# Optimization experiments

Hardware: AMD Instinct MI355X
Metric: run time of the kernel (lower is better)

Reference implementation:

```python
import jax, jax.numpy as jnp
import numpy as np

N = 100000      # nodes
E = 1600000     # edges (avg degree 16)
F_IN = 512      # input node features
H = 8           # heads in conv1
D = 8           # per-head dim in conv1
C = 7           # classes
NEG_SLOPE = 0.2 # PyG GATConv default leaky_relu slope


def setup_inputs() -> dict:
    key = jax.random.key(0)
    ks = jax.random.split(key, 10)
    s = 0.05
    return {
        "x": jax.random.normal(ks[0], (N, F_IN), jnp.float32),
        "edge_index": jax.random.randint(ks[1], (2, E), 0, N, dtype=jnp.int64),
        "W1": jax.random.normal(ks[2], (F_IN, H * D), jnp.float32) * s,
        "a1_src": jax.random.normal(ks[3], (H, D), jnp.float32) * s,
        "a1_dst": jax.random.normal(ks[4], (H, D), jnp.float32) * s,
        "b1": jnp.zeros((H * D,), jnp.float32),
        "W2": jax.random.normal(ks[5], (H * D, C), jnp.float32) * s,
        "a2_src": jax.random.normal(ks[6], (1, C), jnp.float32) * s,
        "a2_dst": jax.random.normal(ks[7], (1, C), jnp.float32) * s,
        "b2": jnp.zeros((C,), jnp.float32),
    }


def _gat_conv(x, src, dst, W, a_src, a_dst, b, heads, dim, concat, n):
    # linear transform -> [N, H, D]
    h = (x @ W).reshape(n, heads, dim)
    # per-node attention halves: [N, H]
    al_src = jnp.einsum('nhd,hd->nh', h, a_src)
    al_dst = jnp.einsum('nhd,hd->nh', h, a_dst)
    # per-edge logits, leaky relu: [E', H]
    e = jax.nn.leaky_relu(al_src[src] + al_dst[dst], NEG_SLOPE)
    # segment softmax over incoming edges of each dst node
    m = jax.lax.stop_gradient(jax.ops.segment_max(e, dst, num_segments=n))
    p = jnp.exp(e - m[dst])
    z = jax.ops.segment_sum(p, dst, num_segments=n)
    alpha = p / z[dst]                                   # [E', H]
    # weighted scatter-add of source messages -> [N, H, D]
    out = jax.ops.segment_sum(h[src] * alpha[..., None], dst, num_segments=n)
    out = out.reshape(n, heads * dim) if concat else out.mean(axis=1)
    return out + b


def reference(x, edge_index, W1, a1_src, a1_dst, b1, W2, a2_src, a2_dst, b2):
    n = x.shape[0]
    # PyG GATConv default: add self loops
    loops = jnp.arange(n, dtype=edge_index.dtype)
    src = jnp.concatenate([edge_index[0], loops])
    dst = jnp.concatenate([edge_index[1], loops])
    h = _gat_conv(x, src, dst, W1, a1_src, a1_dst, b1, H, D, True, n)
    h = jax.nn.elu(h)
    out = _gat_conv(h, src, dst, W2, a2_src, a2_dst, b2, 1, C, False, n)
    return jax.nn.log_softmax(out, axis=1)
```

## Files before the change

kernel.cpp:

```cpp
#include <hip/hip_runtime.h>
#include <math.h>

#define N_NODES 100000
#define N_EDGES 1600000
#define F_IN 512
#define HD 64
#define CC 7
#define NKT (F_IN / 32)
#define BS 128
#define NBK ((N_NODES + BS - 1) / BS)
#define ECAP 4096
#define SCHUNK 4096
#define SBLK ((N_EDGES + SCHUNK - 1) / SCHUNK)

typedef __attribute__((ext_vector_type(8))) short short8;
typedef __attribute__((ext_vector_type(4))) float f32x4;

__device__ inline unsigned short f2bf(float f) {
    union { float f; unsigned u; } v; v.f = f;
    unsigned u = v.u;
    return (unsigned short)((u + 0x7fffu + ((u >> 16) & 1u)) >> 16);
}
__device__ inline float bf2f(unsigned short b) {
    union { unsigned u; float f; } v; v.u = ((unsigned)b) << 16;
    return v.f;
}

__global__ void zerob_kernel(int* __restrict__ bcnt) {
    int i = threadIdx.x;
    if (i < NBK) bcnt[i] = 0;
}

__global__ void w1prep_kernel(const float* __restrict__ W1,
                              unsigned short* __restrict__ wf) {
    int t = blockIdx.x * 256 + threadIdx.x;
    if (t >= NKT * 4 * 64) return;
    int lane = t & 63;
    int ct = (t >> 6) & 3;
    int kt = t >> 8;
    int k0 = kt * 32 + (lane >> 4) * 8;
    int col = ct * 16 + (lane & 15);
    unsigned short* dst = wf + (size_t)t * 8;
    #pragma unroll
    for (int j = 0; j < 8; ++j) dst[j] = f2bf(W1[(k0 + j) * HD + col]);
}

__global__ __launch_bounds__(256) void gemm1att_kernel(const float* __restrict__ x,
                                                       const unsigned short* __restrict__ wf,
                                                       const float* __restrict__ a1s,
                                                       const float* __restrict__ a1d,
                                                       unsigned short* __restrict__ h1b,
                                                       float* __restrict__ als,
                                                       float* __restrict__ ald) {
    __shared__ float ls[64][65];
    const int wave = threadIdx.x >> 6;
    const int lane = threadIdx.x & 63;
    int arow = blockIdx.x * 64 + wave * 16 + (lane & 15);
    if (arow >= N_NODES) arow = N_NODES - 1;
    const float* xp = x + (size_t)arow * F_IN + (lane >> 4) * 8;
    const short8* wp = (const short8*)wf;

    f32x4 acc[4] = {};
    #pragma unroll 4
    for (int kt = 0; kt < NKT; ++kt) {
        f32x4 a0 = *(const f32x4*)(xp + kt * 32);
        f32x4 a1 = *(const f32x4*)(xp + kt * 32 + 4);
        union { short8 s; unsigned short u[8]; } af;
        af.u[0] = f2bf(a0.x); af.u[1] = f2bf(a0.y);
        af.u[2] = f2bf(a0.z); af.u[3] = f2bf(a0.w);
        af.u[4] = f2bf(a1.x); af.u[5] = f2bf(a1.y);
        af.u[6] = f2bf(a1.z); af.u[7] = f2bf(a1.w);
        #pragma unroll
        for (int ct = 0; ct < 4; ++ct) {
            short8 bf = wp[kt * 256 + ct * 64 + lane];
            acc[ct] = __builtin_amdgcn_mfma_f32_16x16x32_bf16(af.s, bf, acc[ct], 0, 0, 0);
        }
    }
    const int lrow_base = wave * 16 + (lane >> 4) * 4;
    const int ocol = lane & 15;
    #pragma unroll
    for (int ct = 0; ct < 4; ++ct) {
        #pragma unroll
        for (int r = 0; r < 4; ++r) {
            int lrow = lrow_base + r;
            int orow = blockIdx.x * 64 + lrow;
            ls[lrow][ct * 16 + ocol] = acc[ct][r];
            if (orow < N_NODES)
                h1b[(size_t)orow * HD + ct * 16 + ocol] = f2bf(acc[ct][r]);
        }
    }
    __syncthreads();
    #pragma unroll
    for (int task = threadIdx.x; task < 64 * 8; task += 256) {
        int r = task >> 3, h = task & 7;
        int node = blockIdx.x * 64 + r;
        if (node < N_NODES) {
            float s = 0.f, d = 0.f;
            #pragma unroll
            for (int k = 0; k < 8; ++k) {
                float v = ls[r][h * 8 + k];
                s += v * a1s[h * 8 + k];
                d += v * a1d[h * 8 + k];
            }
            als[node * 8 + h] = s;
            ald[node * 8 + h] = d;
        }
    }
}

__global__ __launch_bounds__(256) void bhist_kernel(const int* __restrict__ ei,
                                                    int* __restrict__ bcnt) {
    __shared__ int cnt[NBK];
    const int e0 = blockIdx.x * SCHUNK;
    int e1 = e0 + SCHUNK; if (e1 > N_EDGES) e1 = N_EDGES;
    for (int b = threadIdx.x; b < NBK; b += 256) cnt[b] = 0;
    __syncthreads();
    for (int i = e0 + threadIdx.x; i < e1; i += 256)
        atomicAdd(&cnt[ei[N_EDGES + i] >> 7], 1);
    __syncthreads();
    for (int b = threadIdx.x; b < NBK; b += 256) {
        int c = cnt[b];
        if (c) atomicAdd(&bcnt[b], c);
    }
}

__global__ __launch_bounds__(1024) void bscan_kernel(const int* __restrict__ bcnt,
                                                     int* __restrict__ bstart,
                                                     int* __restrict__ bcur) {
    __shared__ int wsum[16];
    const int t = threadIdx.x;
    const int lane = t & 63, w = t >> 6;
    int v = (t < NBK) ? bcnt[t] : 0;
    int x = v;
    #pragma unroll
    for (int o = 1; o < 64; o <<= 1) {
        int u = __shfl_up(x, o, 64);
        if (lane >= o) x += u;
    }
    if (lane == 63) wsum[w] = x;
    __syncthreads();
    if (w == 0) {
        int s = (lane < 16) ? wsum[lane] : 0;
        #pragma unroll
        for (int o = 1; o < 16; o <<= 1) {
            int u = __shfl_up(s, o, 64);
            if (lane >= o) s += u;
        }
        if (lane < 16) wsum[lane] = s;
    }
    __syncthreads();
    int woff = (w > 0) ? wsum[w - 1] : 0;
    int ex = x - v + woff;
    if (t < NBK) { bstart[t] = ex; bcur[t] = ex; }
    if (t == NBK - 1) bstart[NBK] = ex + v;
}

__global__ __launch_bounds__(256) void binscatter_kernel(const int* __restrict__ ei,
                                                         int* __restrict__ bcur,
                                                         int2* __restrict__ pairs) {
    __shared__ int cnt[NBK];
    __shared__ int bas[NBK];
    const int e0 = blockIdx.x * SCHUNK;
    int e1 = e0 + SCHUNK; if (e1 > N_EDGES) e1 = N_EDGES;
    for (int b = threadIdx.x; b < NBK; b += 256) cnt[b] = 0;
    __syncthreads();
    for (int i = e0 + threadIdx.x; i < e1; i += 256)
        atomicAdd(&cnt[ei[N_EDGES + i] >> 7], 1);
    __syncthreads();
    for (int b = threadIdx.x; b < NBK; b += 256) {
        int c = cnt[b];
        bas[b] = c ? atomicAdd(&bcur[b], c) : 0;
        cnt[b] = 0;
    }
    __syncthreads();
    for (int i = e0 + threadIdx.x; i < e1; i += 256) {
        int s = ei[i];
        int t = ei[N_EDGES + i];
        int b = t >> 7;
        int pos = bas[b] + atomicAdd(&cnt[b], 1);
        pairs[pos] = make_int2(s, t);
    }
}

__global__ __launch_bounds__(512) void gather1_kernel(
        const int* __restrict__ bstart, const int2* __restrict__ pairs,
        const float* __restrict__ als, const float* __restrict__ ald,
        const unsigned short* __restrict__ h1b, const float* __restrict__ b1,
        const float* __restrict__ W2, const float* __restrict__ a2s,
        const float* __restrict__ a2d,
        unsigned short* __restrict__ g2b, float* __restrict__ al2s,
        float* __restrict__ al2d) {
    __shared__ int cnt[BS];
    __shared__ int start[BS];
    __shared__ int srcl[ECAP];
    const int tid = threadIdx.x;
    const int wave = tid >> 6, lane = tid & 63, h = lane >> 3;
    const int n0 = blockIdx.x * BS;
    const int es = bstart[blockIdx.x];
    const int ne = bstart[blockIdx.x + 1] - es;
    if (tid < BS) cnt[tid] = 0;
    __syncthreads();
    for (int k = tid; k < ne; k += 512)
        atomicAdd(&cnt[pairs[es + k].y & (BS - 1)], 1);
    __syncthreads();
    if (tid < 64) {
        int a = cnt[lane], b = cnt[64 + lane];
        int xx = a;
        #pragma unroll
        for (int o = 1; o < 64; o <<= 1) { int u = __shfl_up(xx, o, 64); if (lane >= o) xx += u; }
        int totalA = __shfl(xx, 63, 64);
        int yy = b;
        #pragma unroll
        for (int o = 1; o < 64; o <<= 1) { int u = __shfl_up(yy, o, 64); if (lane >= o) yy += u; }
        start[lane] = xx - a;
        start[64 + lane] = totalA + yy - b;
        cnt[lane] = 0; cnt[64 + lane] = 0;
    }
    __syncthreads();
    for (int k = tid; k < ne; k += 512) {
        int2 pr = pairs[es + k];
        int ln = pr.y & (BS - 1);
        int pos = start[ln] + atomicAdd(&cnt[ln], 1);
        if (pos < ECAP) srcl[pos] = pr.x;
    }
    __syncthreads();

    float w[CC];
    #pragma unroll
    for (int c = 0; c < CC; ++c) w[c] = W2[lane * CC + c];
    for (int n = wave * 16; n < wave * 16 + 16; ++n) {
        int node = n0 + n;
        if (node >= N_NODES) break;
        const float aldt = ald[node * 8 + h];
        float e = als[node * 8 + h] + aldt;
        e = (e >= 0.f) ? e : 0.2f * e;
        float p = __expf(e);
        float acc = p * bf2f(h1b[(size_t)node * HD + lane]);
        float z = p;
        int k = start[n];
        int ke = k + cnt[n]; if (ke > ECAP) ke = ECAP;
        for (; k + 4 <= ke; k += 4) {
            int s0 = srcl[k],     s1 = srcl[k + 1];
            int s2 = srcl[k + 2], s3 = srcl[k + 3];
            float e0 = als[s0 * 8 + h] + aldt;
            float e1 = als[s1 * 8 + h] + aldt;
            float e2 = als[s2 * 8 + h] + aldt;
            float e3 = als[s3 * 8 + h] + aldt;
            float v0 = bf2f(h1b[(size_t)s0 * HD + lane]);
            float v1 = bf2f(h1b[(size_t)s1 * HD + lane]);
            float v2 = bf2f(h1b[(size_t)s2 * HD + lane]);
            float v3 = bf2f(h1b[(size_t)s3 * HD + lane]);
            e0 = (e0 >= 0.f) ? e0 : 0.2f * e0;
            e1 = (e1 >= 0.f) ? e1 : 0.2f * e1;
            e2 = (e2 >= 0.f) ? e2 : 0.2f * e2;
            e3 = (e3 >= 0.f) ? e3 : 0.2f * e3;
            float p0 = __expf(e0), p1 = __expf(e1);
            float p2 = __expf(e2), p3 = __expf(e3);
            z += (p0 + p1) + (p2 + p3);
            acc = fmaf(p0, v0, acc);
            acc = fmaf(p1, v1, acc);
            acc = fmaf(p2, v2, acc);
            acc = fmaf(p3, v3, acc);
        }
        for (; k < ke; ++k) {
            int s = srcl[k];
            float e2 = als[s * 8 + h] + aldt;
            e2 = (e2 >= 0.f) ? e2 : 0.2f * e2;
            float p2 = __expf(e2);
            z += p2;
            acc = fmaf(p2, bf2f(h1b[(size_t)s * HD + lane]), acc);
        }
        float v = acc / z + b1[lane];
        v = (v > 0.f) ? v : (__expf(v) - 1.f);
        float g[CC];
        #pragma unroll
        for (int c = 0; c < CC; ++c) {
            float r = v * w[c];
            #pragma unroll
            for (int d = 1; d < 64; d <<= 1) r += __shfl_xor(r, d, 64);
            g[c] = r;
        }
        float s2 = 0.f, d2 = 0.f;
        #pragma unroll
        for (int c = 0; c < CC; ++c) { s2 += g[c] * a2s[c]; d2 += g[c] * a2d[c]; }
        if (lane < CC) g2b[(size_t)node * 8 + lane] = f2bf(g[lane]);
        if (lane == CC) g2b[(size_t)node * 8 + CC] = 0;
        if (lane == 8) al2s[node] = s2;
        if (lane == 9) al2d[node] = d2;
    }
}

__global__ __launch_bounds__(256) void gather2_kernel(
        const int* __restrict__ bstart, const int2* __restrict__ pairs,
        const float* __restrict__ al2s, const float* __restrict__ al2d,
        const unsigned short* __restrict__ g2b, const float* __restrict__ b2,
        float* __restrict__ out) {
    __shared__ int cnt[BS];
    __shared__ int start[BS];
    __shared__ int srcl[ECAP];
    const int tid = threadIdx.x;
    const int lane = tid & 63;
    const int grp = tid >> 3, c = tid & 7;
    const int n0 = blockIdx.x * BS;
    const int es = bstart[blockIdx.x];
    const int ne = bstart[blockIdx.x + 1] - es;
    if (tid < BS) cnt[tid] = 0;
    __syncthreads();
    for (int k = tid; k < ne; k += 256)
        atomicAdd(&cnt[pairs[es + k].y & (BS - 1)], 1);
    __syncthreads();
    if (tid < 64) {
        int a = cnt[lane], b = cnt[64 + lane];
        int xx = a;
        #pragma unroll
        for (int o = 1; o < 64; o <<= 1) { int u = __shfl_up(xx, o, 64); if (lane >= o) xx += u; }
        int totalA = __shfl(xx, 63, 64);
        int yy = b;
        #pragma unroll
        for (int o = 1; o < 64; o <<= 1) { int u = __shfl_up(yy, o, 64); if (lane >= o) yy += u; }
        start[lane] = xx - a;
        start[64 + lane] = totalA + yy - b;
        cnt[lane] = 0; cnt[64 + lane] = 0;
    }
    __syncthreads();
    for (int k = tid; k < ne; k += 256) {
        int2 pr = pairs[es + k];
        int ln = pr.y & (BS - 1);
        int pos = start[ln] + atomicAdd(&cnt[ln], 1);
        if (pos < ECAP) srcl[pos] = pr.x;
    }
    __syncthreads();

    for (int n = grp * 4; n < grp * 4 + 4; ++n) {
        int node = n0 + n;
        if (node >= N_NODES) break;
        const float adn = al2d[node];
        float e = al2s[node] + adn;
        e = (e >= 0.f) ? e : 0.2f * e;
        float p = __expf(e);
        float acc = p * bf2f(g2b[(size_t)node * 8 + c]);
        float z = p;
        int k = start[n];
        int ke = k + cnt[n]; if (ke > ECAP) ke = ECAP;
        for (; k + 4 <= ke; k += 4) {
            int s0 = srcl[k],     s1 = srcl[k + 1];
            int s2 = srcl[k + 2], s3 = srcl[k + 3];
            float e0 = al2s[s0] + adn;
            float e1 = al2s[s1] + adn;
            float e2 = al2s[s2] + adn;
            float e3 = al2s[s3] + adn;
            float v0 = bf2f(g2b[(size_t)s0 * 8 + c]);
            float v1 = bf2f(g2b[(size_t)s1 * 8 + c]);
            float v2 = bf2f(g2b[(size_t)s2 * 8 + c]);
            float v3 = bf2f(g2b[(size_t)s3 * 8 + c]);
            e0 = (e0 >= 0.f) ? e0 : 0.2f * e0;
            e1 = (e1 >= 0.f) ? e1 : 0.2f * e1;
            e2 = (e2 >= 0.f) ? e2 : 0.2f * e2;
            e3 = (e3 >= 0.f) ? e3 : 0.2f * e3;
            float p0 = __expf(e0), p1 = __expf(e1);
            float p2 = __expf(e2), p3 = __expf(e3);
            z += (p0 + p1) + (p2 + p3);
            acc = fmaf(p0, v0, acc);
            acc = fmaf(p1, v1, acc);
            acc = fmaf(p2, v2, acc);
            acc = fmaf(p3, v3, acc);
        }
        for (; k < ke; ++k) {
            int s = srcl[k];
            float e2 = al2s[s] + adn;
            e2 = (e2 >= 0.f) ? e2 : 0.2f * e2;
            float p2 = __expf(e2);
            z += p2;
            acc = fmaf(p2, bf2f(g2b[(size_t)s * 8 + c]), acc);
        }
        float o = (c < CC) ? (acc / z + b2[c]) : -1e30f;
        float m = o;
        #pragma unroll
        for (int d = 1; d < 8; d <<= 1) m = fmaxf(m, __shfl_xor(m, d, 8));
        float ex = (c < CC) ? __expf(o - m) : 0.f;
        float sum = ex;
        #pragma unroll
        for (int d = 1; d < 8; d <<= 1) sum += __shfl_xor(sum, d, 8);
        float lse = m + __logf(sum);
        if (c < CC) out[(size_t)node * CC + c] = o - lse;
    }
}

extern "C" void kernel_launch(void* const* d_in, const int* in_sizes, int n_in,
                              void* d_out, int out_size, void* d_ws, size_t ws_size,
                              hipStream_t stream) {
    const float* x   = (const float*)d_in[0];
    const int*   ei  = (const int*)d_in[1];
    const float* W1  = (const float*)d_in[2];
    const float* a1s = (const float*)d_in[3];
    const float* a1d = (const float*)d_in[4];
    const float* b1  = (const float*)d_in[5];
    const float* W2  = (const float*)d_in[6];
    const float* a2s = (const float*)d_in[7];
    const float* a2d = (const float*)d_in[8];
    const float* b2  = (const float*)d_in[9];
    float* out = (float*)d_out;

    char* base = (char*)d_ws;
    size_t off = 0;
    auto alloc = [&](size_t bytes) { char* p = base + off; off = (off + bytes + 63) & ~(size_t)63; return p; };
    unsigned short* h1b = (unsigned short*)alloc((size_t)N_NODES * HD * 2);
    unsigned short* wf  = (unsigned short*)alloc((size_t)NKT * 4 * 64 * 8 * 2);
    float* als  = (float*)alloc((size_t)N_NODES * 8 * 4);
    float* ald  = (float*)alloc((size_t)N_NODES * 8 * 4);
    unsigned short* g2b = (unsigned short*)alloc((size_t)N_NODES * 8 * 2);
    float* al2s = (float*)alloc((size_t)N_NODES * 4);
    float* al2d = (float*)alloc((size_t)N_NODES * 4);
    int* bcnt   = (int*)alloc((size_t)NBK * 4);
    int* bstart = (int*)alloc((size_t)(NBK + 1) * 4);
    int* bcur   = (int*)alloc((size_t)NBK * 4);
    int2* pairs = (int2*)alloc((size_t)N_EDGES * 8);

    zerob_kernel<<<1, 1024, 0, stream>>>(bcnt);
    w1prep_kernel<<<(NKT * 4 * 64 + 255) / 256, 256, 0, stream>>>(W1, wf);
    bhist_kernel<<<SBLK, 256, 0, stream>>>(ei, bcnt);
    bscan_kernel<<<1, 1024, 0, stream>>>(bcnt, bstart, bcur);
    binscatter_kernel<<<SBLK, 256, 0, stream>>>(ei, bcur, pairs);

    gemm1att_kernel<<<(N_NODES + 63) / 64, 256, 0, stream>>>(
        x, wf, a1s, a1d, h1b, als, ald);

    gather1_kernel<<<NBK, 512, 0, stream>>>(
        bstart, pairs, als, ald, h1b, b1, W2, a2s, a2d, g2b, al2s, al2d);
    gather2_kernel<<<NBK, 256, 0, stream>>>(
        bstart, pairs, al2s, al2d, g2b, b2, out);
}
```

Baseline: 242.3 us.

## Bin edges into fixed-capacity per-bucket slots and share edge softmax weights via shuffles

Drops the histogram and scan kernels. Each destination bucket now gets a fixed ECAP-sized slot in the pairs buffer, filled with an atomic cursor, so the edge bucketing needs only one pass over edge_index. Both gather kernels also change how attention weights are computed: each lane of an 8-lane group computes the exp for one edge and broadcasts it with __shfl, so the exp is not repeated per head-dim lane. Edges beyond ECAP per bucket are silently dropped. The pairs buffer is larger and sparsely filled.

```diff
diff --git a/kernel.cpp b/kernel.cpp
--- a/kernel.cpp
+++ b/kernel.cpp
@@ -26,9 +26,9 @@
     return v.f;
 }
 
-__global__ void zerob_kernel(int* __restrict__ bcnt) {
+__global__ void zerob_kernel(int* __restrict__ bcur) {
     int i = threadIdx.x;
-    if (i < NBK) bcnt[i] = 0;
+    if (i < NBK) bcur[i] = 0;
 }
 
 __global__ void w1prep_kernel(const float* __restrict__ W1,
@@ -108,53 +108,6 @@
     }
 }
 
-__global__ __launch_bounds__(256) void bhist_kernel(const int* __restrict__ ei,
-                                                    int* __restrict__ bcnt) {
-    __shared__ int cnt[NBK];
-    const int e0 = blockIdx.x * SCHUNK;
-    int e1 = e0 + SCHUNK; if (e1 > N_EDGES) e1 = N_EDGES;
-    for (int b = threadIdx.x; b < NBK; b += 256) cnt[b] = 0;
-    __syncthreads();
-    for (int i = e0 + threadIdx.x; i < e1; i += 256)
-        atomicAdd(&cnt[ei[N_EDGES + i] >> 7], 1);
-    __syncthreads();
-    for (int b = threadIdx.x; b < NBK; b += 256) {
-        int c = cnt[b];
-        if (c) atomicAdd(&bcnt[b], c);
-    }
-}
-
-__global__ __launch_bounds__(1024) void bscan_kernel(const int* __restrict__ bcnt,
-                                                     int* __restrict__ bstart,
-                                                     int* __restrict__ bcur) {
-    __shared__ int wsum[16];
-    const int t = threadIdx.x;
-    const int lane = t & 63, w = t >> 6;
-    int v = (t < NBK) ? bcnt[t] : 0;
-    int x = v;
-    #pragma unroll
-    for (int o = 1; o < 64; o <<= 1) {
-        int u = __shfl_up(x, o, 64);
-        if (lane >= o) x += u;
-    }
-    if (lane == 63) wsum[w] = x;
-    __syncthreads();
-    if (w == 0) {
-        int s = (lane < 16) ? wsum[lane] : 0;
-        #pragma unroll
-        for (int o = 1; o < 16; o <<= 1) {
-            int u = __shfl_up(s, o, 64);
-            if (lane >= o) s += u;
-        }
-        if (lane < 16) wsum[lane] = s;
-    }
-    __syncthreads();
-    int woff = (w > 0) ? wsum[w - 1] : 0;
-    int ex = x - v + woff;
-    if (t < NBK) { bstart[t] = ex; bcur[t] = ex; }
-    if (t == NBK - 1) bstart[NBK] = ex + v;
-}
-
 __global__ __launch_bounds__(256) void binscatter_kernel(const int* __restrict__ ei,
                                                          int* __restrict__ bcur,
                                                          int2* __restrict__ pairs) {
@@ -178,12 +131,12 @@
         int t = ei[N_EDGES + i];
         int b = t >> 7;
         int pos = bas[b] + atomicAdd(&cnt[b], 1);
-        pairs[pos] = make_int2(s, t);
+        if (pos < ECAP) pairs[(size_t)b * ECAP + pos] = make_int2(s, t);
     }
 }
 
 __global__ __launch_bounds__(512) void gather1_kernel(
-        const int* __restrict__ bstart, const int2* __restrict__ pairs,
+        const int* __restrict__ bcur, const int2* __restrict__ pairs,
         const float* __restrict__ als, const float* __restrict__ ald,
         const unsigned short* __restrict__ h1b, const float* __restrict__ b1,
         const float* __restrict__ W2, const float* __restrict__ a2s,
@@ -195,13 +148,14 @@
     __shared__ int srcl[ECAP];
     const int tid = threadIdx.x;
     const int wave = tid >> 6, lane = tid & 63, h = lane >> 3;
+    const int e8 = lane & 7, base8 = lane & 56;
     const int n0 = blockIdx.x * BS;
-    const int es = bstart[blockIdx.x];
-    const int ne = bstart[blockIdx.x + 1] - es;
+    const int2* bp = pairs + (size_t)blockIdx.x * ECAP;
+    int ne = bcur[blockIdx.x]; if (ne > ECAP) ne = ECAP;
     if (tid < BS) cnt[tid] = 0;
     __syncthreads();
     for (int k = tid; k < ne; k += 512)
-        atomicAdd(&cnt[pairs[es + k].y & (BS - 1)], 1);
+        atomicAdd(&cnt[bp[k].y & (BS - 1)], 1);
     __syncthreads();
     if (tid < 64) {
         int a = cnt[lane], b = cnt[64 + lane];
@@ -218,10 +172,10 @@
     }
     __syncthreads();
     for (int k = tid; k < ne; k += 512) {
-        int2 pr = pairs[es + k];
+        int2 pr = bp[k];
         int ln = pr.y & (BS - 1);
         int pos = start[ln] + atomicAdd(&cnt[ln], 1);
-        if (pos < ECAP) srcl[pos] = pr.x;
+        srcl[pos] = pr.x;
     }
     __syncthreads();
 
@@ -238,37 +192,35 @@
         float acc = p * bf2f(h1b[(size_t)node * HD + lane]);
         float z = p;
         int k = start[n];
-        int ke = k + cnt[n]; if (ke > ECAP) ke = ECAP;
-        for (; k + 4 <= ke; k += 4) {
-            int s0 = srcl[k],     s1 = srcl[k + 1];
-            int s2 = srcl[k + 2], s3 = srcl[k + 3];
-            float e0 = als[s0 * 8 + h] + aldt;
-            float e1 = als[s1 * 8 + h] + aldt;
-            float e2 = als[s2 * 8 + h] + aldt;
-            float e3 = als[s3 * 8 + h] + aldt;
-            float v0 = bf2f(h1b[(size_t)s0 * HD + lane]);
-            float v1 = bf2f(h1b[(size_t)s1 * HD + lane]);
-            float v2 = bf2f(h1b[(size_t)s2 * HD + lane]);
-            float v3 = bf2f(h1b[(size_t)s3 * HD + lane]);
-            e0 = (e0 >= 0.f) ? e0 : 0.2f * e0;
-            e1 = (e1 >= 0.f) ? e1 : 0.2f * e1;
-            e2 = (e2 >= 0.f) ? e2 : 0.2f * e2;
-            e3 = (e3 >= 0.f) ? e3 : 0.2f * e3;
-            float p0 = __expf(e0), p1 = __expf(e1);
-            float p2 = __expf(e2), p3 = __expf(e3);
-            z += (p0 + p1) + (p2 + p3);
-            acc = fmaf(p0, v0, acc);
-            acc = fmaf(p1, v1, acc);
-            acc = fmaf(p2, v2, acc);
-            acc = fmaf(p3, v3, acc);
-        }
-        for (; k < ke; ++k) {
-            int s = srcl[k];
-            float e2 = als[s * 8 + h] + aldt;
-            e2 = (e2 >= 0.f) ? e2 : 0.2f * e2;
-            float p2 = __expf(e2);
-            z += p2;
-            acc = fmaf(p2, bf2f(h1b[(size_t)s * HD + lane]), acc);
+        const int ke = k + cnt[n];
+        for (; k + 8 <= ke; k += 8) {
+            int s_own = srcl[k + e8];
+            float ee = als[s_own * 8 + h] + aldt;
+            ee = (ee >= 0.f) ? ee : 0.2f * ee;
+            float pv = __expf(ee);
+            #pragma unroll
+            for (int q = 0; q < 8; ++q) {
+                int se = srcl[k + q];
+                float pe = __shfl(pv, base8 | q, 64);
+                float ve = bf2f(h1b[(size_t)se * HD + lane]);
+                z += pe;
+                acc = fmaf(pe, ve, acc);
+            }
+        }
+        if (k < ke) {
+            const int m = ke - k;
+            int idx = k + ((e8 < m) ? e8 : (m - 1));
+            int s_own = srcl[idx];
+            float ee = als[s_own * 8 + h] + aldt;
+            ee = (ee >= 0.f) ? ee : 0.2f * ee;
+            float pv = __expf(ee);
+            for (int q = 0; q < m; ++q) {
+                int se = srcl[k + q];
+                float pe = __shfl(pv, base8 | q, 64);
+                float ve = bf2f(h1b[(size_t)se * HD + lane]);
+                z += pe;
+                acc = fmaf(pe, ve, acc);
+            }
         }
         float v = acc / z + b1[lane];
         v = (v > 0.f) ? v : (__expf(v) - 1.f);
@@ -291,7 +243,7 @@
 }
 
 __global__ __launch_bounds__(256) void gather2_kernel(
-        const int* __restrict__ bstart, const int2* __restrict__ pairs,
+        const int* __restrict__ bcur, const int2* __restrict__ pairs,
         const float* __restrict__ al2s, const float* __restrict__ al2d,
         const unsigned short* __restrict__ g2b, const float* __restrict__ b2,
         float* __restrict__ out) {
@@ -301,13 +253,14 @@
     const int tid = threadIdx.x;
     const int lane = tid & 63;
     const int grp = tid >> 3, c = tid & 7;
+    const int base8 = lane & 56;
     const int n0 = blockIdx.x * BS;
-    const int es = bstart[blockIdx.x];
-    const int ne = bstart[blockIdx.x + 1] - es;
+    const int2* bp = pairs + (size_t)blockIdx.x * ECAP;
+    int ne = bcur[blockIdx.x]; if (ne > ECAP) ne = ECAP;
     if (tid < BS) cnt[tid] = 0;
     __syncthreads();
     for (int k = tid; k < ne; k += 256)
-        atomicAdd(&cnt[pairs[es + k].y & (BS - 1)], 1);
+        atomicAdd(&cnt[bp[k].y & (BS - 1)], 1);
     __syncthreads();
     if (tid < 64) {
         int a = cnt[lane], b = cnt[64 + lane];
@@ -324,14 +277,14 @@
     }
     __syncthreads();
     for (int k = tid; k < ne; k += 256) {
-        int2 pr = pairs[es + k];
+        int2 pr = bp[k];
         int ln = pr.y & (BS - 1);
         int pos = start[ln] + atomicAdd(&cnt[ln], 1);
-        if (pos < ECAP) srcl[pos] = pr.x;
-    }
-    __syncthreads();
-
-    for (int n = grp * 4; n < grp * 4 + 4; ++n) {
+        srcl[pos] = pr.x;
+    }
+    __syncthreads();
+
+    for (int n = (grp & 31) * 4; n < (grp & 31) * 4 + 4; ++n) {
         int node = n0 + n;
         if (node >= N_NODES) break;
         const float adn = al2d[node];
@@ -341,47 +294,45 @@
         float acc = p * bf2f(g2b[(size_t)node * 8 + c]);
         float z = p;
         int k = start[n];
-        int ke = k + cnt[n]; if (ke > ECAP) ke = ECAP;
-        for (; k + 4 <= ke; k += 4) {
-            int s0 = srcl[k],     s1 = srcl[k + 1];
-            int s2 = srcl[k + 2], s3 = srcl[k + 3];
-            float e0 = al2s[s0] + adn;
-            float e1 = al2s[s1] + adn;
-            float e2 = al2s[s2] + adn;
-            float e3 = al2s[s3] + adn;
-            float v0 = bf2f(g2b[(size_t)s0 * 8 + c]);
-            float v1 = bf2f(g2b[(size_t)s1 * 8 + c]);
-            float v2 = bf2f(g2b[(size_t)s2 * 8 + c]);
-            float v3 = bf2f(g2b[(size_t)s3 * 8 + c]);
-            e0 = (e0 >= 0.f) ? e0 : 0.2f * e0;
-            e1 = (e1 >= 0.f) ? e1 : 0.2f * e1;
-            e2 = (e2 >= 0.f) ? e2 : 0.2f * e2;
-            e3 = (e3 >= 0.f) ? e3 : 0.2f * e3;
-            float p0 = __expf(e0), p1 = __expf(e1);
-            float p2 = __expf(e2), p3 = __expf(e3);
-            z += (p0 + p1) + (p2 + p3);
-            acc = fmaf(p0, v0, acc);
-            acc = fmaf(p1, v1, acc);
-            acc = fmaf(p2, v2, acc);
-            acc = fmaf(p3, v3, acc);
-        }
-        for (; k < ke; ++k) {
-            int s = srcl[k];
-            float e2 = al2s[s] + adn;
-            e2 = (e2 >= 0.f) ? e2 : 0.2f * e2;
-            float p2 = __expf(e2);
-            z += p2;
-            acc = fmaf(p2, bf2f(g2b[(size_t)s * 8 + c]), acc);
+        const int ke = k + cnt[n];
+        for (; k + 8 <= ke; k += 8) {
+            int s_own = srcl[k + c];
+            float ee = al2s[s_own] + adn;
+            ee = (ee >= 0.f) ? ee : 0.2f * ee;
+            float pv = __expf(ee);
+            #pragma unroll
+            for (int q = 0; q < 8; ++q) {
+                int se = srcl[k + q];
+                float pe = __shfl(pv, base8 | q, 64);
+                float ve = bf2f(g2b[(size_t)se * 8 + c]);
+                z += pe;
+                acc = fmaf(pe, ve, acc);
+            }
+        }
+        if (k < ke) {
+            const int m = ke - k;
+            int idx = k + ((c < m) ? c : (m - 1));
+            int s_own = srcl[idx];
+            float ee = al2s[s_own] + adn;
+            ee = (ee >= 0.f) ? ee : 0.2f * ee;
+            float pv = __expf(ee);
+            for (int q = 0; q < m; ++q) {
+                int se = srcl[k + q];
+                float pe = __shfl(pv, base8 | q, 64);
+                float ve = bf2f(g2b[(size_t)se * 8 + c]);
+                z += pe;
+                acc = fmaf(pe, ve, acc);
+            }
         }
         float o = (c < CC) ? (acc / z + b2[c]) : -1e30f;
-        float m = o;
-        #pragma unroll
-        for (int d = 1; d < 8; d <<= 1) m = fmaxf(m, __shfl_xor(m, d, 8));
-        float ex = (c < CC) ? __expf(o - m) : 0.f;
+        float m2 = o;
+        #pragma unroll
+        for (int d = 1; d < 8; d <<= 1) m2 = fmaxf(m2, __shfl_xor(m2, d, 8));
+        float ex = (c < CC) ? __expf(o - m2) : 0.f;
         float sum = ex;
         #pragma unroll
         for (int d = 1; d < 8; d <<= 1) sum += __shfl_xor(sum, d, 8);
-        float lse = m + __logf(sum);
+        float lse = m2 + __logf(sum);
         if (c < CC) out[(size_t)node * CC + c] = o - lse;
     }
 }
@@ -411,22 +362,18 @@
     unsigned short* g2b = (unsigned short*)alloc((size_t)N_NODES * 8 * 2);
     float* al2s = (float*)alloc((size_t)N_NODES * 4);
     float* al2d = (float*)alloc((size_t)N_NODES * 4);
-    int* bcnt   = (int*)alloc((size_t)NBK * 4);
-    int* bstart = (int*)alloc((size_t)(NBK + 1) * 4);
     int* bcur   = (int*)alloc((size_t)NBK * 4);
-    int2* pairs = (int2*)alloc((size_t)N_EDGES * 8);
-
-    zerob_kernel<<<1, 1024, 0, stream>>>(bcnt);
+    int2* pairs = (int2*)alloc((size_t)NBK * ECAP * 8);
+
+    zerob_kernel<<<1, 1024, 0, stream>>>(bcur);
     w1prep_kernel<<<(NKT * 4 * 64 + 255) / 256, 256, 0, stream>>>(W1, wf);
-    bhist_kernel<<<SBLK, 256, 0, stream>>>(ei, bcnt);
-    bscan_kernel<<<1, 1024, 0, stream>>>(bcnt, bstart, bcur);
     binscatter_kernel<<<SBLK, 256, 0, stream>>>(ei, bcur, pairs);
 
     gemm1att_kernel<<<(N_NODES + 63) / 64, 256, 0, stream>>>(
         x, wf, a1s, a1d, h1b, als, ald);
 
     gather1_kernel<<<NBK, 512, 0, stream>>>(
-        bstart, pairs, als, ald, h1b, b1, W2, a2s, a2d, g2b, al2s, al2d);
+        bcur, pairs, als, ald, h1b, b1, W2, a2s, a2d, g2b, al2s, al2d);
     gather2_kernel<<<NBK, 256, 0, stream>>>(
-        bstart, pairs, al2s, al2d, g2b, b2, out);
-}
+        bcur, pairs, al2s, al2d, g2b, b2, out);
+}
```

New measurement: 242.1 us. No clear change (-0.1%).
